# Kernel tuning notes

Measured on AMD Instinct MI355X. Metric: run time of the kernel, lower is better.

The kernel has to match this reference:

```python
import jax, jax.numpy as jnp
import numpy as np

GROUP_SIZE = 1024
SHIFT = 512  # int(group_size * shift_ratio), layer_idx=1 -> should_shift
SCALE = 128 ** -0.5  # head_dim ** -0.5


def setup_inputs() -> dict:
    key = jax.random.key(0)
    kq, kk, kv = jax.random.split(key, 3)
    shape = (1, 16, 8192, 128)  # [batch, heads, seq, head_dim]
    return {
        "query": jax.random.normal(kq, shape, dtype=jnp.float32),
        "key": jax.random.normal(kk, shape, dtype=jnp.float32),
        "value": jax.random.normal(kv, shape, dtype=jnp.float32),
    }


def reference(query, key, value):
    b, h, s, d = query.shape
    g = GROUP_SIZE
    ng = s // g  # seq_len chosen divisible by group_size (no padding branch)

    # shift: roll all tensors left by SHIFT along seq (layer_idx is odd)
    q = jnp.roll(query, -SHIFT, axis=2)
    k = jnp.roll(key, -SHIFT, axis=2)
    v = jnp.roll(value, -SHIFT, axis=2)

    # group-local attention: [b, h, ng, g, d]
    q = q.reshape(b, h, ng, g, d)
    k = k.reshape(b, h, ng, g, d)
    v = v.reshape(b, h, ng, g, d)

    scores = jnp.einsum("bhnqd,bhnkd->bhnqk", q, k) * SCALE
    weights = jax.nn.softmax(scores, axis=-1)
    out = jnp.einsum("bhnqk,bhnkd->bhnqd", weights, v)
    out = out.reshape(b, h, s, d)

    # unshift
    out = jnp.roll(out, SHIFT, axis=2)
    return out
```

## Files before the change

kernel.cpp:

```cpp
#include <hip/hip_runtime.h>
#include <hip/hip_bf16.h>

#define S 8192
#define D 128
#define G 1024
#define SHIFTC 512
#define SMASK 8191
#define SCALE 0.08838834764831845f
#define KVB 64
#define NTILE 16
#define QT 128

typedef __attribute__((ext_vector_type(8))) short short8;
typedef __attribute__((ext_vector_type(16))) float f32x16;

__device__ inline short f2bf(float f) {
    __hip_bfloat16 h = __float2bfloat16(f);
    return *(short*)&h;
}
__device__ inline int cvtpk(float lo, float hi) {
    int r;
    asm("v_cvt_pk_bf16_f32 %0, %1, %2" : "=v"(r) : "v"(lo), "v"(hi));
    return r;
}
__device__ inline float vcomp(const float4& v, int dd) {
    switch (dd) { case 0: return v.x; case 1: return v.y; case 2: return v.z; default: return v.w; }
}

__global__ __launch_bounds__(256, 2) void ssattn(
        const float* __restrict__ qg, const float* __restrict__ kg,
        const float* __restrict__ vg, float* __restrict__ og) {
    __shared__ ushort Klds[KVB * D];
    __shared__ ushort Vt[D * KVB];
    __shared__ float lbuf[4][32];

    const int bid = blockIdx.x;
    const int swz = (bid & 7) * 128 + (bid >> 3);
    const int head = swz >> 6;
    const int grp = (swz >> 3) & 7;
    const int qt = swz & 7;

    const int tid = threadIdx.x;
    const int w = tid >> 6;
    const int l = tid & 63;
    const int lq = l & 31;
    const int hi = l >> 5;

    const size_t hb = (size_t)head * S * D;
    const float* qph = qg + hb;
    const float* kph = kg + hb;
    const float* vph = vg + hb;
    float* oph = og + hb;

    const int kbase = grp * G;
    const int qr0 = grp * G + qt * QT + w * 32;

    const int krow = tid >> 4;
    const int kc0 = (tid & 15) * 8;
    const int vk0 = (tid & 7) * 8;
    const int vd0 = (tid >> 3) * 4;

    float4 ka[4][2];
    float4 va[8];

#pragma unroll
    for (int p = 0; p < 4; ++p) {
        int r = (kbase + krow + p * 16 + SHIFTC) & SMASK;
        const float* sp = kph + (size_t)r * D + kc0;
        ka[p][0] = *(const float4*)(sp);
        ka[p][1] = *(const float4*)(sp + 4);
    }
#pragma unroll
    for (int m = 0; m < 8; ++m) {
        int r = (kbase + vk0 + m + SHIFTC) & SMASK;
        va[m] = *(const float4*)(vph + (size_t)r * D + vd0);
    }

    short8 qf[8];
    {
        int qs = (qr0 + lq + SHIFTC) & SMASK;
        const float* qp = qph + (size_t)qs * D + hi * 8;
#pragma unroll
        for (int kk = 0; kk < 8; ++kk) {
            float4 a = *(const float4*)(qp + kk * 16);
            float4 b = *(const float4*)(qp + kk * 16 + 4);
            short8 f;
            f[0] = f2bf(a.x * SCALE); f[1] = f2bf(a.y * SCALE);
            f[2] = f2bf(a.z * SCALE); f[3] = f2bf(a.w * SCALE);
            f[4] = f2bf(b.x * SCALE); f[5] = f2bf(b.y * SCALE);
            f[6] = f2bf(b.z * SCALE); f[7] = f2bf(b.w * SCALE);
            qf[kk] = f;
        }
    }

    f32x16 o[4];
#pragma unroll
    for (int n = 0; n < 4; ++n)
#pragma unroll
        for (int i = 0; i < 16; ++i) o[n][i] = 0.f;
    float l_run = 0.f;

    for (int t = 0; t < NTILE; ++t) {
        __syncthreads();

#pragma unroll
        for (int p = 0; p < 4; ++p) {
            int row = krow + p * 16;
            short8 f;
            f[0] = f2bf(ka[p][0].x); f[1] = f2bf(ka[p][0].y);
            f[2] = f2bf(ka[p][0].z); f[3] = f2bf(ka[p][0].w);
            f[4] = f2bf(ka[p][1].x); f[5] = f2bf(ka[p][1].y);
            f[6] = f2bf(ka[p][1].z); f[7] = f2bf(ka[p][1].w);
            int e = (row * D + kc0) ^ ((row & 7) << 3);
            *(short8*)(&Klds[e]) = f;
        }
#pragma unroll
        for (int dd = 0; dd < 4; ++dd) {
            int d = vd0 + dd;
            short8 f;
#pragma unroll
            for (int m = 0; m < 8; ++m) f[m] = f2bf(vcomp(va[m], dd));
            int e = (d * KVB + vk0) ^ ((d & 7) << 3);
            *(short8*)(&Vt[e]) = f;
        }
        __syncthreads();

        if (t + 1 < NTILE) {
            int kb = kbase + (t + 1) * KVB;
#pragma unroll
            for (int p = 0; p < 4; ++p) {
                int r = (kb + krow + p * 16 + SHIFTC) & SMASK;
                const float* sp = kph + (size_t)r * D + kc0;
                ka[p][0] = *(const float4*)(sp);
                ka[p][1] = *(const float4*)(sp + 4);
            }
        }

        f32x16 st[2];
#pragma unroll
        for (int kr = 0; kr < 2; ++kr)
#pragma unroll
            for (int i = 0; i < 16; ++i) st[kr][i] = 0.f;
#pragma unroll
        for (int kk = 0; kk < 8; ++kk) {
#pragma unroll
            for (int kr = 0; kr < 2; ++kr) {
                int row = kr * 32 + lq;
                int e = (row * D + kk * 16 + hi * 8) ^ ((row & 7) << 3);
                short8 kf = *(const short8*)(&Klds[e]);
                st[kr] = __builtin_amdgcn_mfma_f32_32x32x16_bf16(kf, qf[kk], st[kr], 0, 0, 0);
            }
        }

        if (t + 1 < NTILE) {
            int kb = kbase + (t + 1) * KVB;
#pragma unroll
            for (int m = 0; m < 8; ++m) {
                int r = (kb + vk0 + m + SHIFTC) & SMASK;
                va[m] = *(const float4*)(vph + (size_t)r * D + vd0);
            }
        }

        float ts = 0.f;
#pragma unroll
        for (int kr = 0; kr < 2; ++kr)
#pragma unroll
            for (int r = 0; r < 16; ++r) {
                float e = __expf(st[kr][r]);
                ts += e;
                st[kr][r] = e;
            }
        ts += __shfl_xor(ts, 32);
        l_run += ts;

        short8 pa[4];
#pragma unroll
        for (int ks = 0; ks < 4; ++ks) {
            int base = 8 * (ks & 1);
            int kr = ks >> 1;
            int w0, w1, w2, w3;
            {
                int a = cvtpk(st[kr][base + 0], st[kr][base + 1]);
                int b = cvtpk(st[kr][base + 4], st[kr][base + 5]);
                asm volatile("v_permlane32_swap_b32 %0, %1" : "+v"(a), "+v"(b));
                w0 = a; w2 = b;
            }
            {
                int a = cvtpk(st[kr][base + 2], st[kr][base + 3]);
                int b = cvtpk(st[kr][base + 6], st[kr][base + 7]);
                asm volatile("v_permlane32_swap_b32 %0, %1" : "+v"(a), "+v"(b));
                w1 = a; w3 = b;
            }
            int4 wi = make_int4(w0, w1, w2, w3);
            pa[ks] = *(short8*)(&wi);
        }

#pragma unroll
        for (int n = 0; n < 4; ++n) {
#pragma unroll
            for (int ks = 0; ks < 4; ++ks) {
                int d = 32 * n + lq;
                int e = (d * KVB + ks * 16 + hi * 8) ^ ((d & 7) << 3);
                short8 vf = *(const short8*)(&Vt[e]);
                o[n] = __builtin_amdgcn_mfma_f32_32x32x16_bf16(pa[ks], vf, o[n], 0, 0, 0);
            }
        }
    }

    if (hi == 0) lbuf[w][lq] = l_run;
    __builtin_amdgcn_s_barrier();
#pragma unroll
    for (int r = 0; r < 16; ++r) {
        int qv = (r & 3) + 8 * (r >> 2) + 4 * hi;
        float li = 1.f / lbuf[w][qv];
        int oseq = (qr0 + qv + SHIFTC) & SMASK;
        float* dst = oph + (size_t)oseq * D + lq;
#pragma unroll
        for (int n = 0; n < 4; ++n) dst[n * 32] = o[n][r] * li;
    }
}

extern "C" void kernel_launch(void* const* d_in, const int* in_sizes, int n_in,
                              void* d_out, int out_size, void* d_ws, size_t ws_size,
                              hipStream_t stream) {
    const float* q = (const float*)d_in[0];
    const float* k = (const float*)d_in[1];
    const float* v = (const float*)d_in[2];
    float* o = (float*)d_out;
    ssattn<<<dim3(1024), dim3(256), 0, stream>>>(q, k, v, o);
}
```

Baseline: 277.0 us.

## Use 512-thread blocks with 256-row Q tiles and split K/V staging across waves

Each block now covers 256 query rows with 8 waves, so every K/V tile staged in LDS is shared by twice as many queries. The grid is halved to match. The global-to-LDS staging is split so the low half of threads loads K and the high half loads V, which cuts the per-thread register staging. Softmax now uses exp2 with the log2(e) factor folded into the Q scale, accumulates row sums in four independent partials, and raises wave priority around the MFMA blocks. The risks are higher register pressure under launch_bounds(512,4) and fewer blocks in the grid.

```diff
diff --git a/kernel.cpp b/kernel.cpp
--- a/kernel.cpp
+++ b/kernel.cpp
@@ -6,10 +6,10 @@
 #define G 1024
 #define SHIFTC 512
 #define SMASK 8191
-#define SCALE 0.08838834764831845f
+#define SCALE_L2E 0.12751743232f
 #define KVB 64
 #define NTILE 16
-#define QT 128
+#define QT 256
 
 typedef __attribute__((ext_vector_type(8))) short short8;
 typedef __attribute__((ext_vector_type(16))) float f32x16;
@@ -27,18 +27,18 @@
     switch (dd) { case 0: return v.x; case 1: return v.y; case 2: return v.z; default: return v.w; }
 }
 
-__global__ __launch_bounds__(256, 2) void ssattn(
+__global__ __launch_bounds__(512, 4) void ssattn(
         const float* __restrict__ qg, const float* __restrict__ kg,
         const float* __restrict__ vg, float* __restrict__ og) {
     __shared__ ushort Klds[KVB * D];
     __shared__ ushort Vt[D * KVB];
-    __shared__ float lbuf[4][32];
+    __shared__ float lbuf[8][32];
 
     const int bid = blockIdx.x;
-    const int swz = (bid & 7) * 128 + (bid >> 3);
-    const int head = swz >> 6;
-    const int grp = (swz >> 3) & 7;
-    const int qt = swz & 7;
+    const int swz = (bid & 7) * 64 + (bid >> 3);
+    const int head = swz >> 5;
+    const int grp = (swz >> 2) & 7;
+    const int qt = swz & 3;
 
     const int tid = threadIdx.x;
     const int w = tid >> 6;
@@ -55,25 +55,29 @@
     const int kbase = grp * G;
     const int qr0 = grp * G + qt * QT + w * 32;
 
-    const int krow = tid >> 4;
-    const int kc0 = (tid & 15) * 8;
-    const int vk0 = (tid & 7) * 8;
-    const int vd0 = (tid >> 3) * 4;
-
-    float4 ka[4][2];
-    float4 va[8];
-
-#pragma unroll
-    for (int p = 0; p < 4; ++p) {
-        int r = (kbase + krow + p * 16 + SHIFTC) & SMASK;
-        const float* sp = kph + (size_t)r * D + kc0;
-        ka[p][0] = *(const float4*)(sp);
-        ka[p][1] = *(const float4*)(sp + 4);
-    }
-#pragma unroll
-    for (int m = 0; m < 8; ++m) {
-        int r = (kbase + vk0 + m + SHIFTC) & SMASK;
-        va[m] = *(const float4*)(vph + (size_t)r * D + vd0);
+    const bool wlow = (tid < 256);
+    const int t2 = tid & 255;
+    const int krow = t2 >> 4;
+    const int kc0 = (t2 & 15) * 8;
+    const int vk0 = (t2 & 7) * 8;
+    const int vd0 = (t2 >> 3) * 4;
+
+    float4 stg[8];
+
+    if (wlow) {
+#pragma unroll
+        for (int p = 0; p < 4; ++p) {
+            int r = (kbase + krow + p * 16 + SHIFTC) & SMASK;
+            const float* sp = kph + (size_t)r * D + kc0;
+            stg[2 * p] = *(const float4*)(sp);
+            stg[2 * p + 1] = *(const float4*)(sp + 4);
+        }
+    } else {
+#pragma unroll
+        for (int m = 0; m < 8; ++m) {
+            int r = (kbase + vk0 + m + SHIFTC) & SMASK;
+            stg[m] = *(const float4*)(vph + (size_t)r * D + vd0);
+        }
     }
 
     short8 qf[8];
@@ -85,10 +89,10 @@
             float4 a = *(const float4*)(qp + kk * 16);
             float4 b = *(const float4*)(qp + kk * 16 + 4);
             short8 f;
-            f[0] = f2bf(a.x * SCALE); f[1] = f2bf(a.y * SCALE);
-            f[2] = f2bf(a.z * SCALE); f[3] = f2bf(a.w * SCALE);
-            f[4] = f2bf(b.x * SCALE); f[5] = f2bf(b.y * SCALE);
-            f[6] = f2bf(b.z * SCALE); f[7] = f2bf(b.w * SCALE);
+            f[0] = f2bf(a.x * SCALE_L2E); f[1] = f2bf(a.y * SCALE_L2E);
+            f[2] = f2bf(a.z * SCALE_L2E); f[3] = f2bf(a.w * SCALE_L2E);
+            f[4] = f2bf(b.x * SCALE_L2E); f[5] = f2bf(b.y * SCALE_L2E);
+            f[6] = f2bf(b.z * SCALE_L2E); f[7] = f2bf(b.w * SCALE_L2E);
             qf[kk] = f;
         }
     }
@@ -103,36 +107,47 @@
     for (int t = 0; t < NTILE; ++t) {
         __syncthreads();
 
-#pragma unroll
-        for (int p = 0; p < 4; ++p) {
-            int row = krow + p * 16;
-            short8 f;
-            f[0] = f2bf(ka[p][0].x); f[1] = f2bf(ka[p][0].y);
-            f[2] = f2bf(ka[p][0].z); f[3] = f2bf(ka[p][0].w);
-            f[4] = f2bf(ka[p][1].x); f[5] = f2bf(ka[p][1].y);
-            f[6] = f2bf(ka[p][1].z); f[7] = f2bf(ka[p][1].w);
-            int e = (row * D + kc0) ^ ((row & 7) << 3);
-            *(short8*)(&Klds[e]) = f;
-        }
-#pragma unroll
-        for (int dd = 0; dd < 4; ++dd) {
-            int d = vd0 + dd;
-            short8 f;
-#pragma unroll
-            for (int m = 0; m < 8; ++m) f[m] = f2bf(vcomp(va[m], dd));
-            int e = (d * KVB + vk0) ^ ((d & 7) << 3);
-            *(short8*)(&Vt[e]) = f;
+        if (wlow) {
+#pragma unroll
+            for (int p = 0; p < 4; ++p) {
+                int row = krow + p * 16;
+                short8 f;
+                f[0] = f2bf(stg[2 * p].x); f[1] = f2bf(stg[2 * p].y);
+                f[2] = f2bf(stg[2 * p].z); f[3] = f2bf(stg[2 * p].w);
+                f[4] = f2bf(stg[2 * p + 1].x); f[5] = f2bf(stg[2 * p + 1].y);
+                f[6] = f2bf(stg[2 * p + 1].z); f[7] = f2bf(stg[2 * p + 1].w);
+                int e = (row * D + kc0) ^ ((row & 7) << 3);
+                *(short8*)(&Klds[e]) = f;
+            }
+        } else {
+#pragma unroll
+            for (int dd = 0; dd < 4; ++dd) {
+                int d = vd0 + dd;
+                short8 f;
+#pragma unroll
+                for (int m = 0; m < 8; ++m) f[m] = f2bf(vcomp(stg[m], dd));
+                int e = (d * KVB + vk0) ^ ((d & 7) << 3);
+                *(short8*)(&Vt[e]) = f;
+            }
         }
         __syncthreads();
 
         if (t + 1 < NTILE) {
             int kb = kbase + (t + 1) * KVB;
-#pragma unroll
-            for (int p = 0; p < 4; ++p) {
-                int r = (kb + krow + p * 16 + SHIFTC) & SMASK;
-                const float* sp = kph + (size_t)r * D + kc0;
-                ka[p][0] = *(const float4*)(sp);
-                ka[p][1] = *(const float4*)(sp + 4);
+            if (wlow) {
+#pragma unroll
+                for (int p = 0; p < 4; ++p) {
+                    int r = (kb + krow + p * 16 + SHIFTC) & SMASK;
+                    const float* sp = kph + (size_t)r * D + kc0;
+                    stg[2 * p] = *(const float4*)(sp);
+                    stg[2 * p + 1] = *(const float4*)(sp + 4);
+                }
+            } else {
+#pragma unroll
+                for (int m = 0; m < 8; ++m) {
+                    int r = (kb + vk0 + m + SHIFTC) & SMASK;
+                    stg[m] = *(const float4*)(vph + (size_t)r * D + vd0);
+                }
             }
         }
 
@@ -141,6 +156,7 @@
         for (int kr = 0; kr < 2; ++kr)
 #pragma unroll
             for (int i = 0; i < 16; ++i) st[kr][i] = 0.f;
+        __builtin_amdgcn_s_setprio(1);
 #pragma unroll
         for (int kk = 0; kk < 8; ++kk) {
 #pragma unroll
@@ -151,25 +167,23 @@
                 st[kr] = __builtin_amdgcn_mfma_f32_32x32x16_bf16(kf, qf[kk], st[kr], 0, 0, 0);
             }
         }
-
-        if (t + 1 < NTILE) {
-            int kb = kbase + (t + 1) * KVB;
-#pragma unroll
-            for (int m = 0; m < 8; ++m) {
-                int r = (kb + vk0 + m + SHIFTC) & SMASK;
-                va[m] = *(const float4*)(vph + (size_t)r * D + vd0);
-            }
-        }
-
-        float ts = 0.f;
-#pragma unroll
-        for (int kr = 0; kr < 2; ++kr)
-#pragma unroll
-            for (int r = 0; r < 16; ++r) {
-                float e = __expf(st[kr][r]);
-                ts += e;
-                st[kr][r] = e;
-            }
+        __builtin_amdgcn_s_setprio(0);
+
+        float ts0 = 0.f, ts1 = 0.f, ts2 = 0.f, ts3 = 0.f;
+#pragma unroll
+        for (int kr = 0; kr < 2; ++kr) {
+#pragma unroll
+            for (int r = 0; r < 16; r += 4) {
+                float e0 = __builtin_amdgcn_exp2f(st[kr][r + 0]);
+                float e1 = __builtin_amdgcn_exp2f(st[kr][r + 1]);
+                float e2 = __builtin_amdgcn_exp2f(st[kr][r + 2]);
+                float e3 = __builtin_amdgcn_exp2f(st[kr][r + 3]);
+                st[kr][r + 0] = e0; st[kr][r + 1] = e1;
+                st[kr][r + 2] = e2; st[kr][r + 3] = e3;
+                ts0 += e0; ts1 += e1; ts2 += e2; ts3 += e3;
+            }
+        }
+        float ts = (ts0 + ts1) + (ts2 + ts3);
         ts += __shfl_xor(ts, 32);
         l_run += ts;
 
@@ -195,6 +209,7 @@
             pa[ks] = *(short8*)(&wi);
         }
 
+        __builtin_amdgcn_s_setprio(1);
 #pragma unroll
         for (int n = 0; n < 4; ++n) {
 #pragma unroll
@@ -205,6 +220,7 @@
                 o[n] = __builtin_amdgcn_mfma_f32_32x32x16_bf16(pa[ks], vf, o[n], 0, 0, 0);
             }
         }
+        __builtin_amdgcn_s_setprio(0);
     }
 
     if (hi == 0) lbuf[w][lq] = l_run;
@@ -227,5 +243,5 @@
     const float* k = (const float*)d_in[1];
     const float* v = (const float*)d_in[2];
     float* o = (float*)d_out;
-    ssattn<<<dim3(1024), dim3(256), 0, stream>>>(q, k, v, o);
-}
+    ssattn<<<dim3(512), dim3(512), 0, stream>>>(q, k, v, o);
+}
```

Result: slower. 583.2 us (+110.6%).
